# Performance work log

Hardware: AMD Instinct MI355X
Metric: run time of the kernel (lower is better)

The kernel has to match this reference:

```python
import jax, jax.numpy as jnp
import numpy as np

L = 2      # shared recursion blocks
B = 2
T = 4096
D = 1024
H = 16
DH = D // H
F = 4096
K = 2048   # token-choice capacity (active tokens per sequence)
S = 0.02   # init scale


def setup_inputs() -> dict:
    key = jax.random.key(0)
    ks = jax.random.split(key, 8)
    return {
        "x": jax.random.normal(ks[0], (B, T, D), jnp.float32),
        "router_w": jax.random.normal(ks[1], (D,), jnp.float32) * S,
        "router_b": jnp.zeros((), jnp.float32),
        "ln1_w": jnp.ones((L, D), jnp.float32),
        "ln1_b": jnp.zeros((L, D), jnp.float32),
        "wqkv": jax.random.normal(ks[2], (L, D, 3 * D), jnp.float32) * S,
        "wo": jax.random.normal(ks[3], (L, D, D), jnp.float32) * S,
        "ln2_w": jnp.ones((L, D), jnp.float32),
        "ln2_b": jnp.zeros((L, D), jnp.float32),
        "w1": jax.random.normal(ks[4], (L, D, F), jnp.float32) * S,
        "w2": jax.random.normal(ks[5], (L, F, D), jnp.float32) * S,
        "k": K,
    }


def _ln(x, w, b):
    mu = x.mean(-1, keepdims=True)
    var = ((x - mu) ** 2).mean(-1, keepdims=True)
    return (x - mu) * jax.lax.rsqrt(var + 1e-5) * w + b


def _block(h, ln1w, ln1b, wqkv, wo, ln2w, ln2b, w1, w2):
    # pre-LN MHA + pre-LN MLP transformer block over the active token subset
    Bk, Kk, Dd = h.shape
    y = _ln(h, ln1w, ln1b)
    qkv = jnp.einsum("bkd,de->bke", y, wqkv)          # [B,K,3D]
    q, kk, v = jnp.split(qkv, 3, axis=-1)
    sh = lambda t: t.reshape(Bk, Kk, H, DH).transpose(0, 2, 1, 3)  # [B,H,K,DH]
    q, kk, v = sh(q), sh(kk), sh(v)
    scores = jnp.einsum("bhqd,bhkd->bhqk", q, kk) / jnp.sqrt(jnp.float32(DH))
    att = jax.nn.softmax(scores, axis=-1)
    o = jnp.einsum("bhqk,bhkd->bhqd", att, v).transpose(0, 2, 1, 3).reshape(Bk, Kk, Dd)
    h = h + jnp.einsum("bkd,de->bke", o, wo)
    y = _ln(h, ln2w, ln2b)
    h = h + jnp.einsum("bkf,fd->bkd", jax.nn.gelu(jnp.einsum("bkd,df->bkf", y, w1)), w2)
    return h


def reference(x, router_w, router_b, ln1_w, ln1_b, wqkv, wo, ln2_w, ln2_b, w1, w2, k):
    # --- token-choice router: per-token scalar logit, top-k capacity selection ---
    logits = jnp.einsum("btd,d->bt", x, router_w) + router_b       # [B,T]
    top_v, selected = jax.lax.top_k(logits, k)                     # [B,K]
    gate_w = jax.nn.sigmoid(top_v)[..., None]                      # [B,K,1]
    # --- gather active tokens (torch.gather along dim 1) ---
    top_k_x = jnp.take_along_axis(x, selected[..., None], axis=1)  # [B,K,D]
    # --- shared recursion blocks ---
    h = top_k_x
    for l in range(L):
        h = _block(h, ln1_w[l], ln1_b[l], wqkv[l], wo[l],
                   ln2_w[l], ln2_b[l], w1[l], w2[l])
    h_out = h * gate_w                                             # weighted gating
    # --- scatter_add back into the full sequence ---
    b_idx = jnp.arange(x.shape[0])[:, None]                        # [B,1]
    out = x.at[b_idx, selected].add(h_out)
    return out
```

## Files before the change

### kernel.cpp

```cpp
#include <hip/hip_runtime.h>
#include <cmath>

typedef __bf16 bf16;
typedef __bf16 bf16x2 __attribute__((ext_vector_type(2)));
typedef __bf16 bf16x4 __attribute__((ext_vector_type(4)));
typedef __bf16 bf16x8 __attribute__((ext_vector_type(8)));
typedef float  f32x4  __attribute__((ext_vector_type(4)));

#define AS1(p) ((const __attribute__((address_space(1))) void*)(p))
#define AS3(p) ((__attribute__((address_space(3))) void*)(p))

constexpr int Bc = 2, Tc = 4096, Dc = 1024, Hc = 16, Fc = 4096, Kc = 2048;

__global__ __launch_bounds__(256) void init_kernel(int* __restrict__ slot,
    int* __restrict__ sel, float* __restrict__ gate){
  int i = blockIdx.x * 256 + threadIdx.x;
  slot[i] = -1;
  if (i < Bc * Kc){ sel[i] = i & (Kc - 1); gate[i] = 0.f; }
}

__global__ __launch_bounds__(256) void router_kernel(const float* __restrict__ x,
    const float* __restrict__ rw, const float* __restrict__ rb, float* __restrict__ logits){
  int wv = threadIdx.x >> 6, lane = threadIdx.x & 63;
  int token = blockIdx.x * 4 + wv;
  const float* xr = x + (size_t)token * Dc;
  float s = 0.f;
#pragma unroll
  for (int i = 0; i < 16; i++){ int d = lane + i*64; s += xr[d] * rw[d]; }
#pragma unroll
  for (int m = 32; m; m >>= 1) s += __shfl_xor(s, m);
  if (lane == 0) logits[token] = s + rb[0];
}

__global__ __launch_bounds__(256) void topk_kernel(const float* __restrict__ logits,
    int* __restrict__ slot, int* __restrict__ sel, float* __restrict__ gate){
  __shared__ float lg[Tc];
  int b = blockIdx.x >> 4, seg = blockIdx.x & 15;
  const float* lb = logits + (size_t)b * Tc;
  for (int i = threadIdx.x; i < Tc; i += 256) lg[i] = lb[i];
  __syncthreads();
  int t = seg * 256 + threadIdx.x;
  float v = lg[t];
  int rank = 0;
  for (int j = 0; j < Tc; j++){
    float u = lg[j];
    rank += (u > v) || (u == v && j < t);
  }
  if (rank < Kc){
    sel [b*Kc + rank] = t;
    gate[b*Kc + rank] = 1.f / (1.f + expf(-v));
    slot[b*Tc + t] = rank;
  }
}

__global__ __launch_bounds__(256) void gather_kernel(const float* __restrict__ x,
    const int* __restrict__ sel, float* __restrict__ h){
  int row = blockIdx.x;
  int b = row >> 11;
  int t = sel[row];
  t = (t < 0) ? 0 : (t >= Tc ? Tc - 1 : t);
  const float* xr = x + ((size_t)b * Tc + t) * Dc;
  float* hr = h + (size_t)row * Dc;
  int d = threadIdx.x * 4;
  *(float4*)(hr + d) = *(const float4*)(xr + d);
}

__global__ __launch_bounds__(256) void ln_kernel(const float* __restrict__ h,
    const float* __restrict__ w, const float* __restrict__ bb, bf16* __restrict__ y){
  __shared__ float red[4], red2[4];
  int row = blockIdx.x, t = threadIdx.x;
  int wv = t >> 6, lane = t & 63;
  const float* hr = h + (size_t)row * Dc;
  float4 x4 = *(const float4*)(hr + t*4);
  float s = x4.x + x4.y + x4.z + x4.w;
#pragma unroll
  for (int m = 32; m; m >>= 1) s += __shfl_xor(s, m);
  if (lane == 0) red[wv] = s;
  __syncthreads();
  float mu = (red[0]+red[1]+red[2]+red[3]) * (1.f/Dc);
  float d0 = x4.x-mu, d1 = x4.y-mu, d2 = x4.z-mu, d3 = x4.w-mu;
  float q = d0*d0 + d1*d1 + d2*d2 + d3*d3;
#pragma unroll
  for (int m = 32; m; m >>= 1) q += __shfl_xor(q, m);
  if (lane == 0) red2[wv] = q;
  __syncthreads();
  float var = (red2[0]+red2[1]+red2[2]+red2[3]) * (1.f/Dc);
  float rs = rsqrtf(var + 1e-5f);
  bf16* yr = y + (size_t)row * Dc;
  int d = t * 4;
  float xv[4] = {x4.x, x4.y, x4.z, x4.w};
#pragma unroll
  for (int i = 0; i < 4; i++)
    yr[d+i] = (bf16)((xv[i]-mu) * rs * w[d+i] + bb[d+i]);
}

__global__ __launch_bounds__(256) void transpose_kernel(const float* __restrict__ in,
    bf16* __restrict__ out, int R, int C){
  __shared__ __attribute__((aligned(16))) bf16 tile[64][72];
  int c0 = blockIdx.x * 64, r0 = blockIdx.y * 64;
  int t = threadIdx.x;
#pragma unroll
  for (int i = 0; i < 2; i++){
    int ch = t + i*256;
    int row = ch >> 3, col8 = (ch & 7) * 8;
    const float* src = in + (size_t)(r0+row)*C + c0 + col8;
    float4 a = *(const float4*)src;
    float4 b = *(const float4*)(src + 4);
    bf16x8 v;
    v[0]=(bf16)a.x; v[1]=(bf16)a.y; v[2]=(bf16)a.z; v[3]=(bf16)a.w;
    v[4]=(bf16)b.x; v[5]=(bf16)b.y; v[6]=(bf16)b.z; v[7]=(bf16)b.w;
    *(bf16x8*)&tile[row][col8] = v;
  }
  __syncthreads();
#pragma unroll
  for (int i = 0; i < 2; i++){
    int ch = t + i*256;
    int orow = ch >> 3, oc8 = (ch & 7) * 8;
    bf16x8 v;
#pragma unroll
    for (int j = 0; j < 8; j++) v[j] = tile[oc8+j][orow];
    *(bf16x8*)(out + (size_t)(c0+orow)*R + r0 + oc8) = v;
  }
}

__device__ __forceinline__ float fast_gelu(float v){
  float u = exp2f(v * (1.f + 0.044715f*v*v) * -2.30220772f);
  return v * __builtin_amdgcn_rcpf(1.f + u);
}

__global__ __launch_bounds__(256) void gemm_bt_kernel(
    const bf16* __restrict__ A, const bf16* __restrict__ Bt,
    bf16* __restrict__ Cbf, float* __restrict__ Cf,
    int M, int N, int Kd, int mode)
{
  __shared__ __attribute__((aligned(16))) bf16 As[128*32];
  __shared__ __attribute__((aligned(16))) bf16 Bs[128*32];
  const int tid = threadIdx.x;
  const int wv = tid >> 6, lane = tid & 63;
  const int wm = wv & 1, wn = wv >> 1;
  const int m0 = blockIdx.y * 128, n0 = blockIdx.x * 128;
  f32x4 acc[4][4] = {};

  const bf16* Ag  = A  + (size_t)(m0      + (tid>>2)) * Kd + (tid&3)*8;
  const bf16* Ag2 = A  + (size_t)(m0 + 64 + (tid>>2)) * Kd + (tid&3)*8;
  const bf16* Bg  = Bt + (size_t)(n0      + (tid>>2)) * Kd + (tid&3)*8;
  const bf16* Bg2 = Bt + (size_t)(n0 + 64 + (tid>>2)) * Kd + (tid&3)*8;
  char* AsB = (char*)As;
  char* BsB = (char*)Bs;

  for (int k0 = 0; k0 < Kd; k0 += 32){
    __syncthreads();
    __builtin_amdgcn_global_load_lds(AS1(Ag  + k0), AS3(AsB +        wv*1024), 16, 0, 0);
    __builtin_amdgcn_global_load_lds(AS1(Ag2 + k0), AS3(AsB + 4096 + wv*1024), 16, 0, 0);
    __builtin_amdgcn_global_load_lds(AS1(Bg  + k0), AS3(BsB +        wv*1024), 16, 0, 0);
    __builtin_amdgcn_global_load_lds(AS1(Bg2 + k0), AS3(BsB + 4096 + wv*1024), 16, 0, 0);
    __syncthreads();
    bf16x8 af[4], bfr[4];
    const bf16* Ab = As + (wm*64 + (lane&15))*32 + (lane>>4)*8;
    const bf16* Bb = Bs + (wn*64 + (lane&15))*32 + (lane>>4)*8;
#pragma unroll
    for (int mt = 0; mt < 4; mt++) af[mt]  = *(const bf16x8*)(Ab + mt*16*32);
#pragma unroll
    for (int nt = 0; nt < 4; nt++) bfr[nt] = *(const bf16x8*)(Bb + nt*16*32);
#pragma unroll
    for (int mt = 0; mt < 4; mt++)
#pragma unroll
      for (int nt = 0; nt < 4; nt++)
        acc[mt][nt] = __builtin_amdgcn_mfma_f32_16x16x32_bf16(af[mt], bfr[nt], acc[mt][nt], 0, 0, 0);
  }
#pragma unroll
  for (int mt = 0; mt < 4; mt++){
    int rr0 = m0 + wm*64 + mt*16 + (lane>>4)*4;
#pragma unroll
    for (int nt = 0; nt < 4; nt++){
      int cc = n0 + wn*64 + nt*16 + (lane&15);
#pragma unroll
      for (int r = 0; r < 4; r++){
        float v = acc[mt][nt][r];
        size_t idx = (size_t)(rr0 + r) * N + cc;
        if (mode == 0)      Cbf[idx] = (bf16)v;
        else if (mode == 1) Cf[idx] += v;
        else                Cbf[idx] = (bf16)fast_gelu(v);
      }
    }
  }
}

__global__ __launch_bounds__(256) void gemm_bt64_kernel(
    const bf16* __restrict__ A, const bf16* __restrict__ Bt,
    bf16* __restrict__ Cbf, float* __restrict__ Cf,
    int M, int N, int Kd, int mode)
{
  __shared__ __attribute__((aligned(16))) bf16 As[128*32];
  __shared__ __attribute__((aligned(16))) bf16 Bs[64*32];
  const int tid = threadIdx.x;
  const int wv = tid >> 6, lane = tid & 63;
  const int wm = wv >> 1, wn = wv & 1;
  const int m0 = blockIdx.y * 128, n0 = blockIdx.x * 64;
  f32x4 acc[4][2] = {};

  const bf16* Ag  = A  + (size_t)(m0      + (tid>>2)) * Kd + (tid&3)*8;
  const bf16* Ag2 = A  + (size_t)(m0 + 64 + (tid>>2)) * Kd + (tid&3)*8;
  const bf16* Bg  = Bt + (size_t)(n0      + (tid>>2)) * Kd + (tid&3)*8;
  char* AsB = (char*)As;
  char* BsB = (char*)Bs;

  for (int k0 = 0; k0 < Kd; k0 += 32){
    __syncthreads();
    __builtin_amdgcn_global_load_lds(AS1(Ag  + k0), AS3(AsB +        wv*1024), 16, 0, 0);
    __builtin_amdgcn_global_load_lds(AS1(Ag2 + k0), AS3(AsB + 4096 + wv*1024), 16, 0, 0);
    __builtin_amdgcn_global_load_lds(AS1(Bg  + k0), AS3(BsB +        wv*1024), 16, 0, 0);
    __syncthreads();
    bf16x8 af[4], bfr[2];
    const bf16* Ab = As + (wm*64 + (lane&15))*32 + (lane>>4)*8;
    const bf16* Bb = Bs + (wn*32 + (lane&15))*32 + (lane>>4)*8;
#pragma unroll
    for (int mt = 0; mt < 4; mt++) af[mt]  = *(const bf16x8*)(Ab + mt*16*32);
#pragma unroll
    for (int nt = 0; nt < 2; nt++) bfr[nt] = *(const bf16x8*)(Bb + nt*16*32);
#pragma unroll
    for (int mt = 0; mt < 4; mt++)
#pragma unroll
      for (int nt = 0; nt < 2; nt++)
        acc[mt][nt] = __builtin_amdgcn_mfma_f32_16x16x32_bf16(af[mt], bfr[nt], acc[mt][nt], 0, 0, 0);
  }
#pragma unroll
  for (int mt = 0; mt < 4; mt++){
    int rr0 = m0 + wm*64 + mt*16 + (lane>>4)*4;
#pragma unroll
    for (int nt = 0; nt < 2; nt++){
      int cc = n0 + wn*32 + nt*16 + (lane&15);
#pragma unroll
      for (int r = 0; r < 4; r++){
        float v = acc[mt][nt][r];
        size_t idx = (size_t)(rr0 + r) * N + cc;
        if (mode == 0)      Cbf[idx] = (bf16)v;
        else if (mode == 1) Cf[idx] += v;
        else                Cbf[idx] = (bf16)fast_gelu(v);
      }
    }
  }
}

__global__ __launch_bounds__(256) void flash_kernel(const bf16* __restrict__ qkv, bf16* __restrict__ o){
  __shared__ __attribute__((aligned(16))) bf16 Ks[64][72];
  __shared__ __attribute__((aligned(16))) bf16 Vt[64*64];
  __shared__ __attribute__((aligned(16))) bf16 Pt[4][64][16];
  const int tid = threadIdx.x, wv = tid >> 6, lane = tid & 63;
  const int quad = lane >> 4, l15 = lane & 15;
  const int bid = blockIdx.x;
  const int qt = bid & 31, hh = (bid >> 5) & 15, b = bid >> 9;
  const int q0 = qt * 64;
  const size_t base = (size_t)b * Kc * (3*Dc);
  const float SC2 = 0.125f * 1.44269504f;

  const int sp8 = (tid & 7) * 8;
  const int kr0 = tid >> 3, kr1 = kr0 + 32;
  const int vr0 = (tid >> 3) * 2;
  const int vg = vr0 >> 3, vlo = vr0 & 7, vsw = sp8 >> 3;

  bf16x8 qf[2];
  {
    const bf16* qr = qkv + base + (size_t)(q0 + wv*16 + l15)*(3*Dc) + hh*64 + quad*8;
    qf[0] = *(const bf16x8*)(qr);
    qf[1] = *(const bf16x8*)(qr + 32);
  }

  const bf16* kp0 = qkv + base + (size_t)kr0*(3*Dc) +   Dc + hh*64 + sp8;
  const bf16* kp1 = qkv + base + (size_t)kr1*(3*Dc) +   Dc + hh*64 + sp8;
  const bf16* vp0 = qkv + base + (size_t)vr0*(3*Dc) + 2*Dc + hh*64 + sp8;
  const bf16* vp1 = vp0 + 3*Dc;
  bf16x8 kpre0 = *(const bf16x8*)kp0;
  bf16x8 kpre1 = *(const bf16x8*)kp1;
  bf16x8 vpre0 = *(const bf16x8*)vp0;
  bf16x8 vpre1 = *(const bf16x8*)vp1;
  const int TSTRIDE = 64 * 3 * Dc;

  bf16x8 onesf;
#pragma unroll
  for (int j = 0; j < 8; j++) onesf[j] = (bf16)(l15 == 0 ? 1.f : 0.f);

  f32x4 oacc[4] = {};
  f32x4 oacc5 = {};
  float mrow[4];
#pragma unroll
  for (int r = 0; r < 4; r++) mrow[r] = -1e30f;

  for (int kt = 0; kt < 32; kt++){
    __syncthreads();
    *(bf16x8*)&Ks[kr0][sp8] = kpre0;
    *(bf16x8*)&Ks[kr1][sp8] = kpre1;
#pragma unroll
    for (int j = 0; j < 8; j++){
      bf16x2 pr; pr[0] = vpre0[j]; pr[1] = vpre1[j];
      *(bf16x2*)&Vt[(sp8 + j)*64 + ((vg ^ j ^ vsw) << 3) + vlo] = pr;
    }
    __syncthreads();
    if (kt < 31){
      kp0 += TSTRIDE; kp1 += TSTRIDE; vp0 += TSTRIDE; vp1 += TSTRIDE;
      kpre0 = *(const bf16x8*)kp0;
      kpre1 = *(const bf16x8*)kp1;
      vpre0 = *(const bf16x8*)vp0;
      vpre1 = *(const bf16x8*)vp1;
    }
    f32x4 sacc[4] = {};
    __builtin_amdgcn_s_setprio(1);
#pragma unroll
    for (int nt = 0; nt < 4; nt++)
#pragma unroll
      for (int s = 0; s < 2; s++){
        bf16x8 kf = *(const bf16x8*)&Ks[nt*16 + l15][s*32 + quad*8];
        sacc[nt] = __builtin_amdgcn_mfma_f32_16x16x32_bf16(qf[s], kf, sacc[nt], 0, 0, 0);
      }
    __builtin_amdgcn_s_setprio(0);
    float lm[4];
#pragma unroll
    for (int r = 0; r < 4; r++)
      lm[r] = fmaxf(fmaxf(sacc[0][r], sacc[1][r]), fmaxf(sacc[2][r], sacc[3][r]));
    bool ok = true;
#pragma unroll
    for (int r = 0; r < 4; r++) ok = ok && (lm[r] * SC2 <= mrow[r] + 8.f);
    if (!__all((int)ok)){
#pragma unroll
      for (int r = 0; r < 4; r++){
        float mx = lm[r];
#pragma unroll
        for (int m = 1; m < 16; m <<= 1) mx = fmaxf(mx, __shfl_xor(mx, m));
        float nm = fmaxf(mrow[r], mx * SC2);
        float alpha = exp2f(mrow[r] - nm);
        mrow[r] = nm;
#pragma unroll
        for (int nt = 0; nt < 4; nt++) oacc[nt][r] *= alpha;
        oacc5[r] *= alpha;
      }
    }
#pragma unroll
    for (int nt = 0; nt < 4; nt++){
      bf16x4 w;
#pragma unroll
      for (int r = 0; r < 4; r++) w[r] = (bf16)exp2f(fmaf(sacc[nt][r], SC2, -mrow[r]));
      *(bf16x4*)&Pt[wv][nt*16 + l15][quad*4] = w;
    }
    bf16x8 pf[2];
    {
      bf16x4 t00, t01, t10, t11;
      const bf16* pr0 = &Pt[wv][     quad*8][l15];
      const bf16* pr1 = &Pt[wv][32 + quad*8][l15];
      asm volatile("ds_read_b64_tr_b16 %0, %1"            : "=v"(t00) : "v"(AS3(pr0)) : "memory");
      asm volatile("ds_read_b64_tr_b16 %0, %1 offset:128" : "=v"(t01) : "v"(AS3(pr0)) : "memory");
      asm volatile("ds_read_b64_tr_b16 %0, %1"            : "=v"(t10) : "v"(AS3(pr1)) : "memory");
      asm volatile("ds_read_b64_tr_b16 %0, %1 offset:128" : "=v"(t11) : "v"(AS3(pr1)) : "memory");
      asm volatile("s_waitcnt lgkmcnt(0)" ::: "memory");
      __builtin_amdgcn_sched_barrier(0);
#pragma unroll
      for (int j = 0; j < 4; j++){
        pf[0][j] = t00[j]; pf[0][j+4] = t01[j];
        pf[1][j] = t10[j]; pf[1][j+4] = t11[j];
      }
    }
    __builtin_amdgcn_s_setprio(1);
#pragma unroll
    for (int nt = 0; nt < 4; nt++){
      int d = nt*16 + l15;
      int sw = (d & 7) ^ ((d >> 3) & 7);
#pragma unroll
      for (int s = 0; s < 2; s++){
        bf16x8 vf = *(const bf16x8*)&Vt[d*64 + (((s*4 + quad) ^ sw) << 3)];
        oacc[nt] = __builtin_amdgcn_mfma_f32_16x16x32_bf16(pf[s], vf, oacc[nt], 0, 0, 0);
      }
    }
    oacc5 = __builtin_amdgcn_mfma_f32_16x16x32_bf16(pf[0], onesf, oacc5, 0, 0, 0);
    oacc5 = __builtin_amdgcn_mfma_f32_16x16x32_bf16(pf[1], onesf, oacc5, 0, 0, 0);
    __builtin_amdgcn_s_setprio(0);
  }
#pragma unroll
  for (int r = 0; r < 4; r++){
    float l = __shfl(oacc5[r], lane & 48);
    float inv = __builtin_amdgcn_rcpf(l);
    int row = q0 + wv*16 + quad*4 + r;
#pragma unroll
    for (int nt = 0; nt < 4; nt++)
      o[((size_t)b*Kc + row)*Dc + hh*64 + nt*16 + l15] = (bf16)(oacc[nt][r] * inv);
  }
}

__global__ __launch_bounds__(256) void scatter_kernel(const float* __restrict__ x,
    const float* __restrict__ h, const float* __restrict__ gate,
    const int* __restrict__ slot, float* __restrict__ out){
  int row = blockIdx.x;
  int b = row >> 12;
  int d = threadIdx.x * 4;
  const float* xr = x + (size_t)row * Dc;
  float* orow = out + (size_t)row * Dc;
  int sl = slot[row];
  if (sl >= 0 && sl < Kc){
    float g = gate[b*Kc + sl];
    const float* hr = h + ((size_t)b*Kc + sl) * Dc;
    float4 xv = *(const float4*)(xr + d);
    float4 hv = *(const float4*)(hr + d);
    float4 ov = { xv.x + g*hv.x, xv.y + g*hv.y, xv.z + g*hv.z, xv.w + g*hv.w };
    *(float4*)(orow + d) = ov;
  } else {
    *(float4*)(orow + d) = *(const float4*)(xr + d);
  }
}

extern "C" void kernel_launch(void* const* d_in, const int* in_sizes, int n_in,
                              void* d_out, int out_size, void* d_ws, size_t ws_size,
                              hipStream_t stream)
{
  const float* x        = (const float*)d_in[0];
  const float* router_w = (const float*)d_in[1];
  const float* router_b = (const float*)d_in[2];
  const float* ln1_w    = (const float*)d_in[3];
  const float* ln1_b    = (const float*)d_in[4];
  const float* wqkv     = (const float*)d_in[5];
  const float* wo       = (const float*)d_in[6];
  const float* ln2_w    = (const float*)d_in[7];
  const float* ln2_b    = (const float*)d_in[8];
  const float* w1       = (const float*)d_in[9];
  const float* w2       = (const float*)d_in[10];
  float* out = (float*)d_out;

  char* ws = (char*)d_ws;
  if (ws_size < 84029440u) return;
  float* logits = (float*)(ws + 0);
  int*   slot   = (int*)  (ws + 36864);
  int*   sel    = (int*)  (ws + 73728);
  float* gate   = (float*)(ws + 94208);
  float* h      = (float*)(ws + 114688);
  bf16*  y      = (bf16*) (ws + 16896000);
  bf16*  big    = (bf16*) (ws + 25288704);
  bf16*  wqkvT  = (bf16*) (ws + 58847232);
  bf16*  woT    = (bf16*) (ws + 65142784);
  bf16*  w1T    = (bf16*) (ws + 67244032);
  bf16*  w2T    = (bf16*) (ws + 75636736);

  init_kernel<<<32, 256, 0, stream>>>(slot, sel, gate);
  router_kernel<<<2048, 256, 0, stream>>>(x, router_w, router_b, logits);
  topk_kernel<<<32, 256, 0, stream>>>(logits, slot, sel, gate);
  gather_kernel<<<4096, 256, 0, stream>>>(x, sel, h);

  for (int l = 0; l < 2; l++){
    transpose_kernel<<<dim3(48,16), 256, 0, stream>>>(wqkv + (size_t)l*Dc*3*Dc, wqkvT, Dc, 3*Dc);
    transpose_kernel<<<dim3(16,16), 256, 0, stream>>>(wo   + (size_t)l*Dc*Dc,   woT,   Dc, Dc);
    transpose_kernel<<<dim3(64,16), 256, 0, stream>>>(w1   + (size_t)l*Dc*Fc,   w1T,   Dc, Fc);
    transpose_kernel<<<dim3(16,64), 256, 0, stream>>>(w2   + (size_t)l*Fc*Dc,   w2T,   Fc, Dc);

    ln_kernel<<<4096, 256, 0, stream>>>(h, ln1_w + l*Dc, ln1_b + l*Dc, y);
    gemm_bt_kernel<<<dim3(24,32), 256, 0, stream>>>(y, wqkvT, big, nullptr, 4096, 3*Dc, Dc, 0);
    flash_kernel<<<1024, 256, 0, stream>>>(big, y);
    gemm_bt64_kernel<<<dim3(16,32), 256, 0, stream>>>(y, woT, nullptr, h, 4096, Dc, Dc, 1);
    ln_kernel<<<4096, 256, 0, stream>>>(h, ln2_w + l*Dc, ln2_b + l*Dc, y);
    gemm_bt_kernel<<<dim3(32,32), 256, 0, stream>>>(y, w1T, big, nullptr, 4096, Fc, Dc, 2);
    gemm_bt64_kernel<<<dim3(16,32), 256, 0, stream>>>(big, w2T, nullptr, h, 4096, Dc, Fc, 1);
  }

  scatter_kernel<<<8192, 256, 0, stream>>>(x, h, gate, slot, out);
}
```

Baseline: 979.3 us.

## Deepen GEMM K-tile to 64 with XOR-swizzled LDS, merge transposes and init

Both bf16 GEMM kernels now stage a 64-wide K slice per iteration instead of 32, halving the number of barrier pairs per output tile. The LDS layout is XOR-swizzled by row so the 16-byte fragment reads avoid bank conflicts. Separately, the four per-layer weight transposes are merged into one launch, and the init kernel is folded into the router kernel to cut launch count. The trade-off is twice the LDS per block, which may lower occupancy, and there is still no double buffering.

```diff
diff --git a/kernel.cpp b/kernel.cpp
--- a/kernel.cpp
+++ b/kernel.cpp
@@ -12,15 +12,12 @@
 
 constexpr int Bc = 2, Tc = 4096, Dc = 1024, Hc = 16, Fc = 4096, Kc = 2048;
 
-__global__ __launch_bounds__(256) void init_kernel(int* __restrict__ slot,
-    int* __restrict__ sel, float* __restrict__ gate){
-  int i = blockIdx.x * 256 + threadIdx.x;
-  slot[i] = -1;
-  if (i < Bc * Kc){ sel[i] = i & (Kc - 1); gate[i] = 0.f; }
-}
-
 __global__ __launch_bounds__(256) void router_kernel(const float* __restrict__ x,
-    const float* __restrict__ rw, const float* __restrict__ rb, float* __restrict__ logits){
+    const float* __restrict__ rw, const float* __restrict__ rb, float* __restrict__ logits,
+    int* __restrict__ slot, int* __restrict__ sel, float* __restrict__ gate){
+  int flat = blockIdx.x * 256 + threadIdx.x;
+  if (flat < Bc * Tc) slot[flat] = -1;
+  if (flat < Bc * Kc){ sel[flat] = flat & (Kc - 1); gate[flat] = 0.f; }
   int wv = threadIdx.x >> 6, lane = threadIdx.x & 63;
   int token = blockIdx.x * 4 + wv;
   const float* xr = x + (size_t)token * Dc;
@@ -94,10 +91,9 @@
     yr[d+i] = (bf16)((xv[i]-mu) * rs * w[d+i] + bb[d+i]);
 }
 
-__global__ __launch_bounds__(256) void transpose_kernel(const float* __restrict__ in,
-    bf16* __restrict__ out, int R, int C){
-  __shared__ __attribute__((aligned(16))) bf16 tile[64][72];
-  int c0 = blockIdx.x * 64, r0 = blockIdx.y * 64;
+__device__ __forceinline__ void transpose_tile(const float* __restrict__ in,
+    bf16* __restrict__ out, int R, int C, int bx, int by, bf16 (*tile)[72]){
+  int c0 = bx * 64, r0 = by * 64;
   int t = threadIdx.x;
 #pragma unroll
   for (int i = 0; i < 2; i++){
@@ -123,6 +119,19 @@
   }
 }
 
+__global__ __launch_bounds__(256) void transpose4_kernel(
+    const float* __restrict__ wqkv, const float* __restrict__ wo,
+    const float* __restrict__ w1,   const float* __restrict__ w2,
+    bf16* __restrict__ wqkvT, bf16* __restrict__ woT,
+    bf16* __restrict__ w1T,   bf16* __restrict__ w2T){
+  __shared__ __attribute__((aligned(16))) bf16 tile[64][72];
+  int id = blockIdx.x;
+  if (id < 768)        transpose_tile(wqkv, wqkvT, Dc, 3*Dc, id % 48,        id / 48,        tile);
+  else if (id < 1024){ int t = id - 768;  transpose_tile(wo, woT, Dc, Dc,   t % 16,         t / 16,         tile); }
+  else if (id < 2048){ int t = id - 1024; transpose_tile(w1, w1T, Dc, Fc,   t % 64,         t / 64,         tile); }
+  else               { int t = id - 2048; transpose_tile(w2, w2T, Fc, Dc,   t % 16,         t / 16,         tile); }
+}
+
 __device__ __forceinline__ float fast_gelu(float v){
   float u = exp2f(v * (1.f + 0.044715f*v*v) * -2.30220772f);
   return v * __builtin_amdgcn_rcpf(1.f + u);
@@ -133,40 +142,49 @@
     bf16* __restrict__ Cbf, float* __restrict__ Cf,
     int M, int N, int Kd, int mode)
 {
-  __shared__ __attribute__((aligned(16))) bf16 As[128*32];
-  __shared__ __attribute__((aligned(16))) bf16 Bs[128*32];
+  __shared__ __attribute__((aligned(16))) bf16 As[128*64];
+  __shared__ __attribute__((aligned(16))) bf16 Bs[128*64];
   const int tid = threadIdx.x;
   const int wv = tid >> 6, lane = tid & 63;
   const int wm = wv & 1, wn = wv >> 1;
+  const int quad = lane >> 4, l15 = lane & 15;
   const int m0 = blockIdx.y * 128, n0 = blockIdx.x * 128;
   f32x4 acc[4][4] = {};
 
-  const bf16* Ag  = A  + (size_t)(m0      + (tid>>2)) * Kd + (tid&3)*8;
-  const bf16* Ag2 = A  + (size_t)(m0 + 64 + (tid>>2)) * Kd + (tid&3)*8;
-  const bf16* Bg  = Bt + (size_t)(n0      + (tid>>2)) * Kd + (tid&3)*8;
-  const bf16* Bg2 = Bt + (size_t)(n0 + 64 + (tid>>2)) * Kd + (tid&3)*8;
+  const int arow = tid >> 3;
+  const int acol = ((tid & 7) ^ (arow & 7)) * 8;
+  const bf16* Ag = A  + (size_t)(m0 + arow) * Kd + acol;
+  const bf16* Bg = Bt + (size_t)(n0 + arow) * Kd + acol;
   char* AsB = (char*)As;
   char* BsB = (char*)Bs;
-
-  for (int k0 = 0; k0 < Kd; k0 += 32){
-    __syncthreads();
-    __builtin_amdgcn_global_load_lds(AS1(Ag  + k0), AS3(AsB +        wv*1024), 16, 0, 0);
-    __builtin_amdgcn_global_load_lds(AS1(Ag2 + k0), AS3(AsB + 4096 + wv*1024), 16, 0, 0);
-    __builtin_amdgcn_global_load_lds(AS1(Bg  + k0), AS3(BsB +        wv*1024), 16, 0, 0);
-    __builtin_amdgcn_global_load_lds(AS1(Bg2 + k0), AS3(BsB + 4096 + wv*1024), 16, 0, 0);
-    __syncthreads();
-    bf16x8 af[4], bfr[4];
-    const bf16* Ab = As + (wm*64 + (lane&15))*32 + (lane>>4)*8;
-    const bf16* Bb = Bs + (wn*64 + (lane&15))*32 + (lane>>4)*8;
-#pragma unroll
-    for (int mt = 0; mt < 4; mt++) af[mt]  = *(const bf16x8*)(Ab + mt*16*32);
-#pragma unroll
-    for (int nt = 0; nt < 4; nt++) bfr[nt] = *(const bf16x8*)(Bb + nt*16*32);
-#pragma unroll
-    for (int mt = 0; mt < 4; mt++)
-#pragma unroll
-      for (int nt = 0; nt < 4; nt++)
-        acc[mt][nt] = __builtin_amdgcn_mfma_f32_16x16x32_bf16(af[mt], bfr[nt], acc[mt][nt], 0, 0, 0);
+  const size_t rstep = (size_t)32 * Kd;
+
+  const bf16* Ab = As + (size_t)(wm*64 + l15) * 64;
+  const bf16* Bb = Bs + (size_t)(wn*64 + l15) * 64;
+  const int rx = l15 & 7;
+
+  for (int k0 = 0; k0 < Kd; k0 += 64){
+    __syncthreads();
+#pragma unroll
+    for (int i = 0; i < 4; i++){
+      __builtin_amdgcn_global_load_lds(AS1(Ag + i*rstep + k0), AS3(AsB + i*4096 + wv*1024), 16, 0, 0);
+      __builtin_amdgcn_global_load_lds(AS1(Bg + i*rstep + k0), AS3(BsB + i*4096 + wv*1024), 16, 0, 0);
+    }
+    __syncthreads();
+#pragma unroll
+    for (int s = 0; s < 2; s++){
+      const int ax = ((s*4 + quad) ^ rx) * 8;
+      bf16x8 af[4], bfr[4];
+#pragma unroll
+      for (int mt = 0; mt < 4; mt++) af[mt]  = *(const bf16x8*)(Ab + mt*1024 + ax);
+#pragma unroll
+      for (int nt = 0; nt < 4; nt++) bfr[nt] = *(const bf16x8*)(Bb + nt*1024 + ax);
+#pragma unroll
+      for (int mt = 0; mt < 4; mt++)
+#pragma unroll
+        for (int nt = 0; nt < 4; nt++)
+          acc[mt][nt] = __builtin_amdgcn_mfma_f32_16x16x32_bf16(af[mt], bfr[nt], acc[mt][nt], 0, 0, 0);
+    }
   }
 #pragma unroll
   for (int mt = 0; mt < 4; mt++){
@@ -191,38 +209,50 @@
     bf16* __restrict__ Cbf, float* __restrict__ Cf,
     int M, int N, int Kd, int mode)
 {
-  __shared__ __attribute__((aligned(16))) bf16 As[128*32];
-  __shared__ __attribute__((aligned(16))) bf16 Bs[64*32];
+  __shared__ __attribute__((aligned(16))) bf16 As[128*64];
+  __shared__ __attribute__((aligned(16))) bf16 Bs[64*64];
   const int tid = threadIdx.x;
   const int wv = tid >> 6, lane = tid & 63;
   const int wm = wv >> 1, wn = wv & 1;
+  const int quad = lane >> 4, l15 = lane & 15;
   const int m0 = blockIdx.y * 128, n0 = blockIdx.x * 64;
   f32x4 acc[4][2] = {};
 
-  const bf16* Ag  = A  + (size_t)(m0      + (tid>>2)) * Kd + (tid&3)*8;
-  const bf16* Ag2 = A  + (size_t)(m0 + 64 + (tid>>2)) * Kd + (tid&3)*8;
-  const bf16* Bg  = Bt + (size_t)(n0      + (tid>>2)) * Kd + (tid&3)*8;
+  const int arow = tid >> 3;
+  const int acol = ((tid & 7) ^ (arow & 7)) * 8;
+  const bf16* Ag = A  + (size_t)(m0 + arow) * Kd + acol;
+  const bf16* Bg = Bt + (size_t)(n0 + arow) * Kd + acol;
   char* AsB = (char*)As;
   char* BsB = (char*)Bs;
-
-  for (int k0 = 0; k0 < Kd; k0 += 32){
-    __syncthreads();
-    __builtin_amdgcn_global_load_lds(AS1(Ag  + k0), AS3(AsB +        wv*1024), 16, 0, 0);
-    __builtin_amdgcn_global_load_lds(AS1(Ag2 + k0), AS3(AsB + 4096 + wv*1024), 16, 0, 0);
-    __builtin_amdgcn_global_load_lds(AS1(Bg  + k0), AS3(BsB +        wv*1024), 16, 0, 0);
-    __syncthreads();
-    bf16x8 af[4], bfr[2];
-    const bf16* Ab = As + (wm*64 + (lane&15))*32 + (lane>>4)*8;
-    const bf16* Bb = Bs + (wn*32 + (lane&15))*32 + (lane>>4)*8;
-#pragma unroll
-    for (int mt = 0; mt < 4; mt++) af[mt]  = *(const bf16x8*)(Ab + mt*16*32);
-#pragma unroll
-    for (int nt = 0; nt < 2; nt++) bfr[nt] = *(const bf16x8*)(Bb + nt*16*32);
-#pragma unroll
-    for (int mt = 0; mt < 4; mt++)
-#pragma unroll
-      for (int nt = 0; nt < 2; nt++)
-        acc[mt][nt] = __builtin_amdgcn_mfma_f32_16x16x32_bf16(af[mt], bfr[nt], acc[mt][nt], 0, 0, 0);
+  const size_t rstep = (size_t)32 * Kd;
+
+  const bf16* Ab = As + (size_t)(wm*64 + l15) * 64;
+  const bf16* Bb = Bs + (size_t)(wn*32 + l15) * 64;
+  const int rx = l15 & 7;
+
+  for (int k0 = 0; k0 < Kd; k0 += 64){
+    __syncthreads();
+#pragma unroll
+    for (int i = 0; i < 4; i++)
+      __builtin_amdgcn_global_load_lds(AS1(Ag + i*rstep + k0), AS3(AsB + i*4096 + wv*1024), 16, 0, 0);
+#pragma unroll
+    for (int i = 0; i < 2; i++)
+      __builtin_amdgcn_global_load_lds(AS1(Bg + i*rstep + k0), AS3(BsB + i*4096 + wv*1024), 16, 0, 0);
+    __syncthreads();
+#pragma unroll
+    for (int s = 0; s < 2; s++){
+      const int ax = ((s*4 + quad) ^ rx) * 8;
+      bf16x8 af[4], bfr[2];
+#pragma unroll
+      for (int mt = 0; mt < 4; mt++) af[mt]  = *(const bf16x8*)(Ab + mt*1024 + ax);
+#pragma unroll
+      for (int nt = 0; nt < 2; nt++) bfr[nt] = *(const bf16x8*)(Bb + nt*1024 + ax);
+#pragma unroll
+      for (int mt = 0; mt < 4; mt++)
+#pragma unroll
+        for (int nt = 0; nt < 2; nt++)
+          acc[mt][nt] = __builtin_amdgcn_mfma_f32_16x16x32_bf16(af[mt], bfr[nt], acc[mt][nt], 0, 0, 0);
+    }
   }
 #pragma unroll
   for (int mt = 0; mt < 4; mt++){
@@ -436,16 +466,15 @@
   bf16*  w1T    = (bf16*) (ws + 67244032);
   bf16*  w2T    = (bf16*) (ws + 75636736);
 
-  init_kernel<<<32, 256, 0, stream>>>(slot, sel, gate);
-  router_kernel<<<2048, 256, 0, stream>>>(x, router_w, router_b, logits);
+  router_kernel<<<2048, 256, 0, stream>>>(x, router_w, router_b, logits, slot, sel, gate);
   topk_kernel<<<32, 256, 0, stream>>>(logits, slot, sel, gate);
   gather_kernel<<<4096, 256, 0, stream>>>(x, sel, h);
 
   for (int l = 0; l < 2; l++){
-    transpose_kernel<<<dim3(48,16), 256, 0, stream>>>(wqkv + (size_t)l*Dc*3*Dc, wqkvT, Dc, 3*Dc);
-    transpose_kernel<<<dim3(16,16), 256, 0, stream>>>(wo   + (size_t)l*Dc*Dc,   woT,   Dc, Dc);
-    transpose_kernel<<<dim3(64,16), 256, 0, stream>>>(w1   + (size_t)l*Dc*Fc,   w1T,   Dc, Fc);
-    transpose_kernel<<<dim3(16,64), 256, 0, stream>>>(w2   + (size_t)l*Fc*Dc,   w2T,   Fc, Dc);
+    transpose4_kernel<<<3072, 256, 0, stream>>>(
+        wqkv + (size_t)l*Dc*3*Dc, wo + (size_t)l*Dc*Dc,
+        w1 + (size_t)l*Dc*Fc,     w2 + (size_t)l*Fc*Dc,
+        wqkvT, woT, w1T, w2T);
 
     ln_kernel<<<4096, 256, 0, stream>>>(h, ln1_w + l*Dc, ln1_b + l*Dc, y);
     gemm_bt_kernel<<<dim3(24,32), 256, 0, stream>>>(y, wqkvT, big, nullptr, 4096, 3*Dc, Dc, 0);
```

New measurement: 877.0 us. 10.4% less time.
